# Kernel optimization log

Hardware: AMD Instinct MI355X
Metric: run time of the kernel (lower is better)

## Reference

```python
import jax, jax.numpy as jnp
import numpy as np

HEADS = 5 - 1  # 4 attention heads (GPSConv heads=4)


def _bn(x, g, b, eps=1e-5):
    # BatchNorm1d, training-mode math (biased variance), matches torch normalization
    mu = x.mean(0)
    var = x.var(0)
    return g * (x - mu) * jax.lax.rsqrt(var + eps) + b


def _forward(x, t, freqs, t_fc1_W, t_fc1_b, t_fc2_W, t_fc2_b, node_W, node_b,
             tproj_W, tproj_b, tcat_W, tcat_b, pen_g, pen_b, pel_W, pel_b,
             cat_W, cat_b, conv_Wg, gru_Wih, gru_bih, gru_Whh, gru_bhh,
             attn_Wqkv, attn_bqkv, attn_Wo, attn_bo, bn_g, bn_b,
             mlp_W1, mlp_b1, mlp_W2, mlp_b2, out_W, out_b):
    B, C, Hh, Ww = x.shape
    HD = node_W.shape[1]          # hidden_dim = 64
    DH = HD // HEADS              # per-head dim = 16
    WL = pen_g.shape[0]           # walk_length = 20

    xf = x.reshape(B, -1)                              # [B, D]
    h = xf @ node_W + node_b                           # node_proj

    # TimeEmbedding: t @ freqs -> sin/cos -> MLP, then time_proj
    tp = t.reshape(B, 1) * freqs.reshape(1, -1)        # [B, nf]
    two_pi = jnp.asarray(2.0 * np.pi, x.dtype)
    te = jnp.concatenate([jnp.sin(two_pi * tp), jnp.cos(two_pi * tp)], axis=-1)
    te = jax.nn.silu(te @ t_fc1_W + t_fc1_b) @ t_fc2_W + t_fc2_b
    h_time = te @ tproj_W + tproj_b
    h = jnp.concatenate([h, h_time], axis=-1) @ tcat_W + tcat_b  # time_cat_proj

    # Fully-connected graph incl. self-loops: A = 1 everywhere, deg = B.
    # Random-walk PE: P = A/deg has all entries 1/B; P is idempotent (P@P = P),
    # hence diag(P^k) = diag(P) = 1/B for every k in 1..walk_length.
    A = jnp.ones((B, B), x.dtype)
    P = A / A.sum(1, keepdims=True)
    pe = jnp.broadcast_to(jnp.diagonal(P)[:, None], (B, WL))
    pe = _bn(pe, pen_g, pen_b)                         # pe_norm (batch stats)
    h = jnp.concatenate([h, pe @ pel_W + pel_b], axis=-1) @ cat_W + cat_b

    inv_sqrt = jnp.asarray(1.0 / np.sqrt(DH), x.dtype)
    for l in range(conv_Wg.shape[0]):                  # 5 GPSConv layers
        # --- GatedGraphConv (num_layers=1): message, add-aggregate, GRU ---
        m = A @ (h @ conv_Wg[l])                       # sum of messages from all src nodes
        gi = m @ gru_Wih[l] + gru_bih[l]               # [B, 3H]
        gh = h @ gru_Whh[l] + gru_bhh[l]
        ir, iz, inn = jnp.split(gi, 3, axis=-1)
        hr, hz, hn = jnp.split(gh, 3, axis=-1)
        r = jax.nn.sigmoid(ir + hr)
        z = jax.nn.sigmoid(iz + hz)
        n = jnp.tanh(inn + r * hn)
        hc = (1.0 - z) * n + z * h                     # GRUCell output
        h1 = _bn(hc + h, bn_g[l, 0], bn_b[l, 0])       # residual + norm1

        # --- global multihead self-attention over the single dense batch ---
        qkv = h @ attn_Wqkv[l] + attn_bqkv[l]
        q, k, v = jnp.split(qkv, 3, axis=-1)
        q = q.reshape(B, HEADS, DH).transpose(1, 0, 2)  # [h, B, d]
        k = k.reshape(B, HEADS, DH).transpose(1, 0, 2)
        v = v.reshape(B, HEADS, DH).transpose(1, 0, 2)
        att = jax.nn.softmax(jnp.einsum('hqd,hkd->hqk', q, k) * inv_sqrt, axis=-1)
        o = jnp.einsum('hqk,hkd->hqd', att, v).transpose(1, 0, 2).reshape(B, HD)
        o = o @ attn_Wo[l] + attn_bo[l]
        h2 = _bn(o + h, bn_g[l, 1], bn_b[l, 1])        # residual + norm2

        s = h1 + h2
        s = s + (jax.nn.relu(s @ mlp_W1[l] + mlp_b1[l]) @ mlp_W2[l] + mlp_b2[l])
        h = _bn(s, bn_g[l, 2], bn_b[l, 2])             # norm3

    return (h @ out_W + out_b).reshape(B, C, Hh, Ww)


def setup_inputs() -> dict:
    key = jax.random.key(0)
    B, C, H, W = 2048, 4, 32, 32
    D = C * H * W                 # 4096
    HD, PE, WL, L = 64, 16, 20, 5
    NF, TH, TC = 8, 64, 64
    ks = iter(jax.random.split(key, 40))

    def rn(shape, s=0.05):
        return jax.random.normal(next(ks), shape, jnp.float32) * s

    return {
        'x': jax.random.normal(next(ks), (B, C, H, W), jnp.float32),
        't': jax.random.uniform(next(ks), (B,), jnp.float32),
        'freqs': rn((NF,), 1.0),
        't_fc1_W': rn((2 * NF, TH)), 't_fc1_b': rn((TH,)),
        't_fc2_W': rn((TH, TC)), 't_fc2_b': rn((TC,)),
        'node_W': rn((D, HD), 0.02), 'node_b': rn((HD,)),
        'tproj_W': rn((TC, HD)), 'tproj_b': rn((HD,)),
        'tcat_W': rn((2 * HD, HD)), 'tcat_b': rn((HD,)),
        'pen_g': jnp.ones((WL,), jnp.float32), 'pen_b': jnp.zeros((WL,), jnp.float32),
        'pel_W': rn((WL, PE)), 'pel_b': rn((PE,)),
        'cat_W': rn((HD + PE, HD)), 'cat_b': rn((HD,)),
        'conv_Wg': rn((L, HD, HD)),
        'gru_Wih': rn((L, HD, 3 * HD)), 'gru_bih': rn((L, 3 * HD)),
        'gru_Whh': rn((L, HD, 3 * HD)), 'gru_bhh': rn((L, 3 * HD)),
        'attn_Wqkv': rn((L, HD, 3 * HD)), 'attn_bqkv': rn((L, 3 * HD)),
        'attn_Wo': rn((L, HD, HD)), 'attn_bo': rn((L, HD)),
        'bn_g': jnp.ones((L, 3, HD), jnp.float32), 'bn_b': jnp.zeros((L, 3, HD), jnp.float32),
        'mlp_W1': rn((L, HD, 2 * HD)), 'mlp_b1': rn((L, 2 * HD)),
        'mlp_W2': rn((L, 2 * HD, HD)), 'mlp_b2': rn((L, HD)),
        'out_W': rn((HD, D)), 'out_b': rn((D,)),
    }


def reference(x, t, freqs, t_fc1_W, t_fc1_b, t_fc2_W, t_fc2_b, node_W, node_b,
              tproj_W, tproj_b, tcat_W, tcat_b, pen_g, pen_b, pel_W, pel_b,
              cat_W, cat_b, conv_Wg, gru_Wih, gru_bih, gru_Whh, gru_bhh,
              attn_Wqkv, attn_bqkv, attn_Wo, attn_bo, bn_g, bn_b,
              mlp_W1, mlp_b1, mlp_W2, mlp_b2, out_W, out_b):
    return _forward(x, t, freqs, t_fc1_W, t_fc1_b, t_fc2_W, t_fc2_b, node_W, node_b,
                    tproj_W, tproj_b, tcat_W, tcat_b, pen_g, pen_b, pel_W, pel_b,
                    cat_W, cat_b, conv_Wg, gru_Wih, gru_bih, gru_Whh, gru_bhh,
                    attn_Wqkv, attn_bqkv, attn_Wo, attn_bo, bn_g, bn_b,
                    mlp_W1, mlp_b1, mlp_W2, mlp_b2, out_W, out_b)
```

## Files before the change

kernel.cpp:

```cpp
#include <hip/hip_runtime.h>

#define NB 2048
#define HDM 64
#define NLAY 5
#define NBLK 1024
#define REP 16

#define BAR_U32 (257*32)
#define HSUMR_F  (REP*NLAY*64)
#define BNACCR_F (REP*NLAY*384)

typedef __bf16 bf16x8 __attribute__((ext_vector_type(8)));
typedef float v4f __attribute__((ext_vector_type(4)));

__device__ __forceinline__ float sigmoidf_(float x){ return 1.f/(1.f+__expf(-x)); }
__device__ __forceinline__ float tanhfast_(float x){
  x = fminf(fmaxf(x, -15.f), 15.f);
  float e = __expf(2.f*x);
  return (e-1.f)/(e+1.f);
}
__device__ __forceinline__ unsigned short f2b_rne(float f){
  unsigned u = __float_as_uint(f);
  unsigned r = u + 0x7FFFu + ((u>>16)&1u);
  return (unsigned short)(r>>16);
}
__device__ __forceinline__ unsigned pk2(float a, float b){
  unsigned ua = (__float_as_uint(a) + 0x8000u) >> 16;
  unsigned ub = (__float_as_uint(b) + 0x8000u) & 0xFFFF0000u;
  return ua | ub;
}


__device__ __forceinline__ float ld_f32_sc(const float* p){
  float v;
  asm volatile("global_load_dword %0, %1, off sc0 sc1\n"
               "s_waitcnt vmcnt(0)"
               : "=v"(v) : "v"(p) : "memory");
  return v;
}
__device__ __forceinline__ void ld4_f32_sc(float& a, float& b, float& c, float& d,
                                           const float* p0, const float* p1,
                                           const float* p2, const float* p3){
  asm volatile("global_load_dword %0, %4, off sc0 sc1\n"
               "global_load_dword %1, %5, off sc0 sc1\n"
               "global_load_dword %2, %6, off sc0 sc1\n"
               "global_load_dword %3, %7, off sc0 sc1\n"
               "s_waitcnt vmcnt(0)"
               : "=&v"(a), "=&v"(b), "=&v"(c), "=&v"(d)
               : "v"(p0), "v"(p1), "v"(p2), "v"(p3) : "memory");
}
__device__ __forceinline__ void st_f32_sc(float* p, float v){
  asm volatile("global_store_dword %0, %1, off sc0 sc1" :: "v"(p), "v"(v) : "memory");
}
__device__ __forceinline__ void st_v4f_sc(float* p, v4f v){
  asm volatile("global_store_dwordx4 %0, %1, off sc0 sc1" :: "v"(p), "v"(v) : "memory");
}
__device__ __forceinline__ void st_u16_sc(unsigned short* p, unsigned short v){
  unsigned vv = v;
  asm volatile("global_store_short %0, %1, off sc0 sc1" :: "v"(p), "v"(vv) : "memory");
}


struct KArgs {
  const float *x, *tt, *freqs, *fc1W, *fc1b, *fc2W, *fc2b, *nodeW, *nodeb,
              *tprojW, *tprojb, *tcatW, *tcatb, *penb, *pelW, *pelb, *catW, *catb,
              *convWg, *gruWih, *grubih, *gruWhh, *grubhh, *Wqkv, *bqkv, *Wo, *bo,
              *bng, *bnb, *W1, *b1, *W2, *b2, *outW, *outb;
  float *htime, *hbuf, *s1, *s2, *smlp, *o_out, *h0p, *out;
  float *hsumR, *bnaccR;
  unsigned short *Qb, *Kb, *Vt;
  unsigned *bar;
};

union SMem {
  struct { float xs[16*260]; float tb0[128]; float tb1[128]; } pre;
  struct { float sa[128]; float sb[128]; float cvec[64]; } as;
  struct { float sa[128]; float tot3[128]; } a;
  struct { unsigned short Pl[4*640]; float Os[4*272]; float ms[64]; float ls[64]; } at;
  struct { float sa[128]; float os[128]; float smv[64]; float smT[64]; float sgi[192];
           float Sb1[128]; float Sb2[128]; } b2;
  struct { float sa[128]; float totC[256]; float sh[2*128]; float S2[128]; } c;
  struct { float hsT[64*12]; float totO[128]; } o;
};

__device__ __forceinline__ void gsync(unsigned* base, unsigned round){
  asm volatile("s_waitcnt vmcnt(0)" ::: "memory");
  __syncthreads();
  if (threadIdx.x == 0){
    const unsigned g = (unsigned)blockIdx.x >> 3;
    unsigned* grp   = base + g*32;
    unsigned* glob  = base + 128*32;
    unsigned* flags = base + 129*32;
    unsigned old = __hip_atomic_fetch_add(grp, 1u, __ATOMIC_RELAXED, __HIP_MEMORY_SCOPE_AGENT);
    if ((old & 7u) == 7u){
      unsigned go = __hip_atomic_fetch_add(glob, 1u, __ATOMIC_RELAXED, __HIP_MEMORY_SCOPE_AGENT);
      if ((go & 127u) == 127u){
        #pragma unroll 8
        for (int i=0;i<128;++i)
          __hip_atomic_store(flags + i*32, round+1u, __ATOMIC_RELAXED, __HIP_MEMORY_SCOPE_AGENT);
      }
    }
    unsigned spins = 0u;
    while (__hip_atomic_load(flags + g*32, __ATOMIC_RELAXED, __HIP_MEMORY_SCOPE_AGENT) < round+1u){
      __builtin_amdgcn_s_sleep(8);
      if (++spins > 200000u) break;
    }
    asm volatile("" ::: "memory");
  }
  __syncthreads();
}

__global__ __launch_bounds__(256, 4) void k_fused(KArgs A)
{
  __shared__ SMem sm;
  __shared__ float ghp[2*192];
  const int t = threadIdx.x;
  const int b = blockIdx.x;
  unsigned rnd = 0;

  {
    const int r = t>>6, c = t&63;
    if (r < 2){
      const int row = b*2 + r;
      const float tv = A.tt[row];
      float te[16];
      #pragma unroll
      for (int j=0;j<8;++j){
        float sv, cv;
        __sincosf(6.28318530717958647692f*tv*A.freqs[j], &sv, &cv);
        te[j]=sv; te[j+8]=cv;
      }
      float a = A.fc1b[c];
      #pragma unroll
      for (int j=0;j<16;++j) a += te[j]*A.fc1W[j*64+c];
      sm.pre.tb0[r*64+c] = a*sigmoidf_(a);
    }
    __syncthreads();
    if (r < 2){
      float b2v = A.fc2b[c];
      #pragma unroll 8
      for (int k=0;k<64;++k) b2v += sm.pre.tb0[r*64+k]*A.fc2W[k*64+c];
      sm.pre.tb1[r*64+c] = b2v;
    }
    __syncthreads();
    if (r < 2){
      const int row = b*2 + r;
      float hti = A.tprojb[c];
      #pragma unroll 8
      for (int k=0;k<64;++k) hti += sm.pre.tb1[r*64+k]*A.tprojW[k*64+c];
      A.htime[row*64+c] = hti;
    }
  }
  {
    const int rg = b>>3, kq = b&7;
    const int rows0 = rg*16, k0 = kq*512;
    const int col4 = (t&15)*4;
    const int rq4  = ((t>>4)&3)*4;
    const int ksub = (t>>6)*64;

    float4 a0={0,0,0,0}, a1={0,0,0,0}, a2={0,0,0,0}, a3={0,0,0,0};

    for (int ch=0; ch<2; ++ch){
      __syncthreads();
      #pragma unroll
      for (int i=0;i<4;++i){
        int fi = t + 256*i;
        int xr = fi>>6, kk = (fi&63)<<2;
        *(float4*)&sm.pre.xs[xr*260+kk] =
            *(const float4*)&A.x[(size_t)(rows0+xr)*4096 + k0 + ch*256 + kk];
      }
      __syncthreads();
      const float* wp = &A.nodeW[(size_t)(k0 + ch*256 + ksub)*64 + col4];
      const float* xp = &sm.pre.xs[rq4*260 + ksub];
      #pragma unroll 8
      for (int kk=0; kk<64; ++kk){
        float4 w  = *(const float4*)&wp[kk*64];
        float x0 = xp[kk];
        float x1 = xp[260+kk];
        float x2 = xp[520+kk];
        float x3 = xp[780+kk];
        a0.x += x0*w.x; a0.y += x0*w.y; a0.z += x0*w.z; a0.w += x0*w.w;
        a1.x += x1*w.x; a1.y += x1*w.y; a1.z += x1*w.z; a1.w += x1*w.w;
        a2.x += x2*w.x; a2.y += x2*w.y; a2.z += x2*w.z; a2.w += x2*w.w;
        a3.x += x3*w.x; a3.y += x3*w.y; a3.z += x3*w.z; a3.w += x3*w.w;
      }
    }
    __syncthreads();
    {
      const int kqi = t>>6;
      *(float4*)&sm.pre.xs[(kqi*16 + rq4 + 0)*64 + col4] = a0;
      *(float4*)&sm.pre.xs[(kqi*16 + rq4 + 1)*64 + col4] = a1;
      *(float4*)&sm.pre.xs[(kqi*16 + rq4 + 2)*64 + col4] = a2;
      *(float4*)&sm.pre.xs[(kqi*16 + rq4 + 3)*64 + col4] = a3;
    }
    __syncthreads();
    {
      const int row = t>>4, c4 = (t&15)*4;
      float4 s = {0,0,0,0};
      #pragma unroll
      for (int q=0;q<4;++q){
        float4 v = *(const float4*)&sm.pre.xs[(q*16+row)*64 + c4];
        s.x+=v.x; s.y+=v.y; s.z+=v.z; s.w+=v.w;
      }
      v4f sv = {s.x, s.y, s.z, s.w};
      st_v4f_sc(&A.h0p[(size_t)kq*(NB*HDM) + (rows0+row)*64 + c4], sv);
    }
  }
  gsync(A.bar, rnd++);

  {
    const int r = t>>6, c = t&63;
    const int row = b*2 + r;
    if (r==0){
      float pl[16];
      #pragma unroll
      for (int j=0;j<16;++j){
        float a = A.pelb[j];
        for (int w=0;w<20;++w) a += A.penb[w]*A.pelW[w*16+j];
        pl[j]=a;
      }
      float a = A.catb[c];
      #pragma unroll
      for (int j=0;j<16;++j) a += pl[j]*A.catW[(64+j)*64+c];
      sm.as.cvec[c]=a;
    }
    if (r < 2){
      float p0,p1,p2,p3,p4,p5,p6,p7;
      ld4_f32_sc(p0,p1,p2,p3,
                 &A.h0p[(size_t)0*(NB*HDM) + row*64 + c], &A.h0p[(size_t)1*(NB*HDM) + row*64 + c],
                 &A.h0p[(size_t)2*(NB*HDM) + row*64 + c], &A.h0p[(size_t)3*(NB*HDM) + row*64 + c]);
      ld4_f32_sc(p4,p5,p6,p7,
                 &A.h0p[(size_t)4*(NB*HDM) + row*64 + c], &A.h0p[(size_t)5*(NB*HDM) + row*64 + c],
                 &A.h0p[(size_t)6*(NB*HDM) + row*64 + c], &A.h0p[(size_t)7*(NB*HDM) + row*64 + c]);
      sm.as.sa[t] = A.nodeb[c] + (((p0+p1)+(p2+p3)) + ((p4+p5)+(p6+p7)));
      sm.as.sb[t] = A.htime[row*64+c];
    }
    __syncthreads();
    float a = 0.f;
    if (r < 2){
      a = A.tcatb[c];
      #pragma unroll 4
      for (int k=0;k<64;++k){
        a += sm.as.sa[r*64+k]*A.tcatW[k*64+c];
        a += sm.as.sb[r*64+k]*A.tcatW[(64+k)*64+c];
      }
    }
    __syncthreads();
    if (r < 2) sm.as.sa[t] = a;
    __syncthreads();
    if (r < 2){
      float hv = sm.as.cvec[c];
      #pragma unroll 8
      for (int k=0;k<64;++k) hv += sm.as.sa[r*64+k]*A.catW[k*64+c];
      A.hbuf[row*64+c] = hv;
    }
  }

  for (int l=0; l<NLAY; ++l){
    const float* gPrev = (l==0) ? A.bng : A.bng + (l-1)*192 + 128;
    const float* bPrev = (l==0) ? A.bnb : A.bnb + (l-1)*192 + 128;
    const float* Whh = A.gruWhh + l*12288;
    const float* bhh = A.grubhh + l*192;
    const float* Wq  = A.Wqkv + l*12288;
    const float* bqv = A.bqkv + l*192;
    const int rep = b & (REP-1);

    __syncthreads();
    {
      const int row0 = b*2;
      if (l>0 && t<128){
        float s = 0.f;
        #pragma unroll
        for (int rp=0;rp<REP;++rp) s += A.bnaccR[rp*1920 + (l-1)*384 + 256 + t];
        sm.a.tot3[t] = s;
      }
      __syncthreads();
      if (t < 128){
        const int rl = t>>6, c = t&63;
        const int row = row0 + rl;
        float hv;
        if (l==0){
          hv = A.hbuf[row*64+c];
        } else {
          float mu = sm.a.tot3[c]*(1.f/NB);
          float va = sm.a.tot3[64+c]*(1.f/NB) - mu*mu;
          float sv = ld_f32_sc(&A.smlp[row*64+c]);
          hv = gPrev[c]*(sv-mu)*rsqrtf(va+1e-5f)+bPrev[c];
          A.hbuf[row*64+c] = hv;
        }
        sm.a.sa[t] = hv;
      }
      __syncthreads();
      if (t<64){
        float s = sm.a.sa[t] + sm.a.sa[64+t];
        atomicAdd(&A.hsumR[rep*320 + l*64 + t], s);
      }
      if (t < 192){
        const int cc = t;
        float ag[2], aq[2];
        float bh = bhh[cc], bq_ = bqv[cc];
        ag[0]=bh; ag[1]=bh; aq[0]=bq_; aq[1]=bq_;
        #pragma unroll 4
        for (int k=0;k<64;++k){
          float wh = Whh[k*192+cc];
          float wq = Wq [k*192+cc];
          float h0 = sm.a.sa[k], h1 = sm.a.sa[64+k];
          ag[0] += h0*wh; ag[1] += h1*wh;
          aq[0] += h0*wq; aq[1] += h1*wq;
        }
        ghp[cc]     = ag[0];
        ghp[192+cc] = ag[1];
        #pragma unroll
        for (int rl2=0;rl2<2;++rl2){
          int rw = row0 + rl2;
          float aqv = aq[rl2];
          if (cc < 64){
            int hd = cc>>4, dh = cc&15;
            size_t base = ((size_t)(hd<<11) + rw)*32;
            st_u16_sc(&A.Qb[base+dh], f2b_rne(aqv*0.25f));
            if (l==0) st_u16_sc(&A.Qb[base+16+dh], (unsigned short)0);
          } else if (cc < 128){
            int c2 = cc-64, hd = c2>>4, dh = c2&15;
            size_t base = ((size_t)(hd<<11) + rw)*32;
            st_u16_sc(&A.Kb[base+dh], f2b_rne(aqv));
            if (l==0) st_u16_sc(&A.Kb[base+16+dh], (unsigned short)0);
          } else {
            int c2 = cc-128, hd = c2>>4, dh = c2&15;
            st_u16_sc(&A.Vt[((size_t)(hd*16+dh))*2048 + rw], f2b_rne(aqv));
          }
        }
      }
    }
    gsync(A.bar, rnd++);

    if (b < 512){
      const int w = t>>6, lane = t&63;
      const int q15 = lane & 15, quad = lane >> 4;
      const int qt = b & 127, head = b>>7;
      const int qrow = qt*16 + q15;
      const int key00 = w*512;
      unsigned short* Plw = &sm.at.Pl[w*640];

      const bf16x8 qf = *(const bf16x8*)&A.Qb[(((size_t)(head<<11))+qrow)*32 + quad*8];
      const unsigned short* Kb_h = A.Kb + ((size_t)(head<<11))*32;
      const unsigned short* Vrow = A.Vt + ((size_t)(head*16+q15))*2048;

      v4f O = {0.f,0.f,0.f,0.f};
      float m = -1e30f, lsum = 0.f;

      bf16x8 kf0 = *(const bf16x8*)&Kb_h[(size_t)(key00 + q15)*32 + quad*8];
      bf16x8 kf1 = *(const bf16x8*)&Kb_h[(size_t)(key00 + 16 + q15)*32 + quad*8];
      bf16x8 vf  = *(const bf16x8*)&Vrow[key00 + quad*8];

      for (int c=0; c<16; ++c){
        bf16x8 nk0, nk1, nv;
        if (c < 15){
          int nk = key00 + (c+1)*32;
          nk0 = *(const bf16x8*)&Kb_h[(size_t)(nk + q15)*32 + quad*8];
          nk1 = *(const bf16x8*)&Kb_h[(size_t)(nk + 16 + q15)*32 + quad*8];
          nv  = *(const bf16x8*)&Vrow[nk + quad*8];
        }
        v4f z = {0.f,0.f,0.f,0.f};
        v4f s0 = __builtin_amdgcn_mfma_f32_16x16x32_bf16(kf0, qf, z, 0,0,0);
        v4f s1 = __builtin_amdgcn_mfma_f32_16x16x32_bf16(kf1, qf, z, 0,0,0);
        float cmax = fmaxf(fmaxf(fmaxf(s0[0],s0[1]),fmaxf(s0[2],s0[3])),
                           fmaxf(fmaxf(s1[0],s1[1]),fmaxf(s1[2],s1[3])));
        cmax = fmaxf(cmax, __shfl_xor(cmax,16,64));
        cmax = fmaxf(cmax, __shfl_xor(cmax,32,64));
        float mnew = fmaxf(m, cmax);
        float alpha = __expf(m - mnew);
        float p0=__expf(s0[0]-mnew), p1=__expf(s0[1]-mnew), p2=__expf(s0[2]-mnew), p3=__expf(s0[3]-mnew);
        float p4=__expf(s1[0]-mnew), p5=__expf(s1[1]-mnew), p6=__expf(s1[2]-mnew), p7=__expf(s1[3]-mnew);
        lsum = alpha*lsum + ((p0+p1)+(p2+p3)+((p4+p5)+(p6+p7)));
        m = mnew;
        O[0]*=alpha; O[1]*=alpha; O[2]*=alpha; O[3]*=alpha;
        *(uint2*)&Plw[q15*40 + quad*4]      = make_uint2(pk2(p0,p1), pk2(p2,p3));
        *(uint2*)&Plw[q15*40 + 16 + quad*4] = make_uint2(pk2(p4,p5), pk2(p6,p7));
        asm volatile("s_waitcnt lgkmcnt(0)" ::: "memory");
        bf16x8 pf = *(const bf16x8*)&Plw[q15*40 + quad*8];
        O = __builtin_amdgcn_mfma_f32_16x16x32_bf16(vf, pf, O, 0,0,0);
        kf0 = nk0; kf1 = nk1; vf = nv;
      }
      lsum += __shfl_xor(lsum,16,64);
      lsum += __shfl_xor(lsum,32,64);
      #pragma unroll
      for (int j=0;j<4;++j) sm.at.Os[w*272 + q15*17 + quad*4 + j] = O[j];
      if (quad==0){ sm.at.ms[w*16+q15]=m; sm.at.ls[w*16+q15]=lsum; }
      __syncthreads();
      {
        const int dh = t&15, q = t>>4;
        float m0=sm.at.ms[q], m1=sm.at.ms[16+q], m2=sm.at.ms[32+q], m3=sm.at.ms[48+q];
        float mm = fmaxf(fmaxf(m0,m1),fmaxf(m2,m3));
        float a0=__expf(m0-mm), a1=__expf(m1-mm), a2=__expf(m2-mm), a3=__expf(m3-mm);
        float ll = a0*sm.at.ls[q]+a1*sm.at.ls[16+q]+a2*sm.at.ls[32+q]+a3*sm.at.ls[48+q];
        float oo = a0*sm.at.Os[q*17+dh] + a1*sm.at.Os[272+q*17+dh]
                 + a2*sm.at.Os[544+q*17+dh] + a3*sm.at.Os[816+q*17+dh];
        st_f32_sc(&A.o_out[(size_t)(qt*16+q)*64 + head*16 + dh], oo / ll);
      }
    }
    gsync(A.bar, rnd++);

    {
      const float* Wg  = A.convWg + l*4096;
      const float* Wih = A.gruWih + l*12288;
      const float* bih = A.grubih + l*192;
      const float* WoL = A.Wo + l*4096;
      const float* boL = A.bo + l*64;
      const int row0 = b*2;

      if (t<64){
        float s = 0.f;
        #pragma unroll
        for (int rp=0;rp<REP;++rp) s += A.hsumR[rp*320 + l*64 + t];
        sm.b2.smT[t] = s;
      }
      if (t<128){
        const int rl = t>>6, c = t&63;
        sm.b2.sa[t] = A.hbuf[(size_t)(row0+rl)*64+c];
        sm.b2.os[t] = ld_f32_sc(&A.o_out[(size_t)(row0+rl)*64+c]);
      }
      __syncthreads();
      if (t<64){
        float a=0.f;
        #pragma unroll 8
        for (int k=0;k<64;++k) a += sm.b2.smT[k]*Wg[k*64+t];
        sm.b2.smv[t]=a;
      }
      __syncthreads();
      if (t<192){
        float a = bih[t];
        #pragma unroll 8
        for (int k=0;k<64;++k) a += sm.b2.smv[k]*Wih[k*192+t];
        sm.b2.sgi[t]=a;
      }
      __syncthreads();
      if (t<128){
        const int c = t&63, rg = t>>6;
        float o2 = boL[c];
        #pragma unroll 4
        for (int k=0;k<64;++k) o2 += sm.b2.os[rg*64+k]*WoL[k*64+c];
        const int row = row0 + rg;
        float hv = sm.b2.sa[rg*64+c];
        float s2v = o2 + hv;
        float ir = sm.b2.sgi[c]      + ghp[rg*192+c];
        float iz = sm.b2.sgi[64+c]   + ghp[rg*192+64+c];
        float inn = sm.b2.sgi[128+c];
        float hn  = ghp[rg*192+128+c];
        float rr_ = sigmoidf_(ir);
        float zz  = sigmoidf_(iz);
        float nn  = tanhfast_(inn + rr_*hn);
        float s1v = (1.f-zz)*nn + zz*hv + hv;
        A.s1[(size_t)row*64+c] = s1v;
        A.s2[(size_t)row*64+c] = s2v;
        sm.b2.Sb1[rg*64+c] = s1v;
        sm.b2.Sb2[rg*64+c] = s2v;
      }
      __syncthreads();
      if (t<64){
        float a = sm.b2.Sb1[t] + sm.b2.Sb1[64+t];
        float aq = sm.b2.Sb1[t]*sm.b2.Sb1[t] + sm.b2.Sb1[64+t]*sm.b2.Sb1[64+t];
        float bb = sm.b2.Sb2[t] + sm.b2.Sb2[64+t];
        float bq2 = sm.b2.Sb2[t]*sm.b2.Sb2[t] + sm.b2.Sb2[64+t]*sm.b2.Sb2[64+t];
        float* bl = &A.bnaccR[rep*1920 + l*384];
        atomicAdd(&bl[t],a);      atomicAdd(&bl[64+t],aq);
        atomicAdd(&bl[128+t],bb); atomicAdd(&bl[192+t],bq2);
      }
    }
    gsync(A.bar, rnd++);

    {
      const float* bngL = A.bng + l*192;
      const float* bnbL = A.bnb + l*192;
      const float* W1l = A.W1 + l*8192;
      const float* b1l = A.b1 + l*128;
      const float* W2l = A.W2 + l*8192;
      const float* b2l = A.b2 + l*64;
      const int row0 = b*2;

      {
        float s = 0.f;
        #pragma unroll
        for (int rp=0;rp<REP;++rp) s += A.bnaccR[rp*1920 + l*384 + t];
        sm.c.totC[t] = s;
      }
      __syncthreads();
      if (t<128){
        const int rl = t>>6, c = t&63;
        const int row = row0 + rl;
        float mu1 = sm.c.totC[c]*(1.f/NB);
        float va1 = sm.c.totC[64+c]*(1.f/NB) - mu1*mu1;
        float mu2 = sm.c.totC[128+c]*(1.f/NB);
        float va2 = sm.c.totC[192+c]*(1.f/NB) - mu2*mu2;
        float h1 = bngL[c]*(A.s1[(size_t)row*64+c]-mu1)*rsqrtf(va1+1e-5f)+bnbL[c];
        float h2 = bngL[64+c]*(A.s2[(size_t)row*64+c]-mu2)*rsqrtf(va2+1e-5f)+bnbL[64+c];
        sm.c.sa[t] = h1+h2;
      }
      __syncthreads();
      {
        const int hj = t&127, rgq = t>>7;
        float a0v=b1l[hj];
        #pragma unroll 4
        for (int k=0;k<64;++k) a0v += sm.c.sa[rgq*64+k]*W1l[k*128+hj];
        sm.c.sh[rgq*128+hj] = fmaxf(a0v,0.f);
      }
      __syncthreads();
      if (t<128){
        const int c = t&63, rg = t>>6;
        float mo = b2l[c];
        #pragma unroll 4
        for (int k=0;k<128;++k) mo += sm.c.sh[rg*128+k]*W2l[k*64+c];
        float smv2 = sm.c.sa[rg*64+c] + mo;
        st_f32_sc(&A.smlp[(size_t)(row0+rg)*64+c], smv2);
        sm.c.S2[rg*64+c] = smv2;
      }
      __syncthreads();
      if (t<64){
        float v0 = sm.c.S2[t], v1 = sm.c.S2[64+t];
        float* bl = &A.bnaccR[rep*1920 + l*384];
        atomicAdd(&bl[256+t], v0+v1);
        atomicAdd(&bl[320+t], v0*v0+v1*v1);
      }
    }
    gsync(A.bar, rnd++);
  }

  {
    const float* g4 = A.bng + 896;
    const float* b4 = A.bnb + 896;
    const int rg = b>>2, cg = b&3;
    const int rows0 = rg*8;
    if (t<128){
      float s = 0.f;
      #pragma unroll
      for (int rp=0;rp<REP;++rp) s += A.bnaccR[rp*1920 + 4*384 + 256 + t];
      sm.o.totO[t] = s;
    }
    __syncthreads();
    #pragma unroll
    for (int i=0;i<2;++i){
      int idx = t + 256*i;
      int k = idx&63, rr = idx>>6;
      float sv = ld_f32_sc(&A.smlp[(size_t)(rows0+rr)*64+k]);
      float mu = sm.o.totO[k]*(1.f/NB);
      float va = sm.o.totO[64+k]*(1.f/NB)-mu*mu;
      sm.o.hsT[k*12+rr] = g4[k]*(sv-mu)*rsqrtf(va+1e-5f)+b4[k];
    }
    __syncthreads();
    const int cc = cg*1024 + t*4;
    float4 acc[8];
    {
      float4 bv = *(const float4*)&A.outb[cc];
      #pragma unroll
      for (int rr=0;rr<8;++rr) acc[rr]=bv;
    }
    #pragma unroll 4
    for (int k=0;k<64;++k){
      float4 w = *(const float4*)&A.outW[(size_t)k*4096+cc];
      const float4* hp = (const float4*)&sm.o.hsT[k*12];
      float4 h0=hp[0], h1=hp[1];
      acc[0].x+=h0.x*w.x;  acc[0].y+=h0.x*w.y;  acc[0].z+=h0.x*w.z;  acc[0].w+=h0.x*w.w;
      acc[1].x+=h0.y*w.x;  acc[1].y+=h0.y*w.y;  acc[1].z+=h0.y*w.z;  acc[1].w+=h0.y*w.w;
      acc[2].x+=h0.z*w.x;  acc[2].y+=h0.z*w.y;  acc[2].z+=h0.z*w.z;  acc[2].w+=h0.z*w.w;
      acc[3].x+=h0.w*w.x;  acc[3].y+=h0.w*w.y;  acc[3].z+=h0.w*w.z;  acc[3].w+=h0.w*w.w;
      acc[4].x+=h1.x*w.x;  acc[4].y+=h1.x*w.y;  acc[4].z+=h1.x*w.z;  acc[4].w+=h1.x*w.w;
      acc[5].x+=h1.y*w.x;  acc[5].y+=h1.y*w.y;  acc[5].z+=h1.y*w.z;  acc[5].w+=h1.y*w.w;
      acc[6].x+=h1.z*w.x;  acc[6].y+=h1.z*w.y;  acc[6].z+=h1.z*w.z;  acc[6].w+=h1.z*w.w;
      acc[7].x+=h1.w*w.x;  acc[7].y+=h1.w*w.y;  acc[7].z+=h1.w*w.z;  acc[7].w+=h1.w*w.w;
    }
    #pragma unroll
    for (int rr=0;rr<8;++rr)
      *(float4*)&A.out[(size_t)(rows0+rr)*4096+cc] = acc[rr];
  }
}


extern "C" void kernel_launch(void* const* d_in, const int* in_sizes, int n_in,
                              void* d_out, int out_size, void* d_ws, size_t ws_size,
                              hipStream_t stream)
{
  (void)in_sizes; (void)n_in; (void)out_size; (void)ws_size;
  KArgs A;
  A.x      = (const float*)d_in[0];
  A.tt     = (const float*)d_in[1];
  A.freqs  = (const float*)d_in[2];
  A.fc1W   = (const float*)d_in[3];
  A.fc1b   = (const float*)d_in[4];
  A.fc2W   = (const float*)d_in[5];
  A.fc2b   = (const float*)d_in[6];
  A.nodeW  = (const float*)d_in[7];
  A.nodeb  = (const float*)d_in[8];
  A.tprojW = (const float*)d_in[9];
  A.tprojb = (const float*)d_in[10];
  A.tcatW  = (const float*)d_in[11];
  A.tcatb  = (const float*)d_in[12];
  A.penb   = (const float*)d_in[14];
  A.pelW   = (const float*)d_in[15];
  A.pelb   = (const float*)d_in[16];
  A.catW   = (const float*)d_in[17];
  A.catb   = (const float*)d_in[18];
  A.convWg = (const float*)d_in[19];
  A.gruWih = (const float*)d_in[20];
  A.grubih = (const float*)d_in[21];
  A.gruWhh = (const float*)d_in[22];
  A.grubhh = (const float*)d_in[23];
  A.Wqkv   = (const float*)d_in[24];
  A.bqkv   = (const float*)d_in[25];
  A.Wo     = (const float*)d_in[26];
  A.bo     = (const float*)d_in[27];
  A.bng    = (const float*)d_in[28];
  A.bnb    = (const float*)d_in[29];
  A.W1     = (const float*)d_in[30];
  A.b1     = (const float*)d_in[31];
  A.W2     = (const float*)d_in[32];
  A.b2     = (const float*)d_in[33];
  A.outW   = (const float*)d_in[34];
  A.outb   = (const float*)d_in[35];

  float* ws = (float*)d_ws;
  A.htime = ws;
  A.hbuf  = A.htime + 131072;
  float* ghRegion = A.hbuf + 131072;
  A.s1    = ghRegion + 393216;
  A.s2    = A.s1 + 131072;
  A.smlp  = A.s2 + 131072;
  A.o_out = A.smlp + 131072;
  float* hsum_legacy = A.o_out + 131072;
  float* bnacc_legacy = hsum_legacy + 320;
  A.Qb = (unsigned short*)(bnacc_legacy + 1920);
  A.Kb = A.Qb + 262144;
  unsigned short* vt_legacy = A.Kb + 262144;
  A.h0p  = (float*)(vt_legacy + 65536);
  A.out  = (float*)d_out;

  A.bar    = (unsigned*)ghRegion;
  A.hsumR  = ghRegion + BAR_U32;
  A.bnaccR = A.hsumR + HSUMR_F;
  A.Vt     = (unsigned short*)(A.bnaccR + BNACCR_F);

  hipMemsetAsync(A.bar, 0, (BAR_U32 + HSUMR_F + BNACCR_F)*sizeof(unsigned), stream);
  k_fused<<<dim3(NBLK), dim3(256), 0, stream>>>(A);
}
```

Baseline: 544.6 us.

## Split attention keys across all blocks and replace grid barrier with per-group flags

Attention now runs on all 1024 blocks instead of 512, each block handling half of the keys and writing partial outputs with max and sum stats. The grid-wide barrier between attention and the GRU/out-projection phase is removed. Each block signals a per-query-tile flag and later spins only on the flags of the tiles it needs, then merges the two partial softmax results itself. This aims to halve attention latency per block and drop one global sync per layer. The cost is an extra partial-merge step, more workspace, and a spin-wait with a bounded timeout.

```diff
diff --git a/kernel.cpp b/kernel.cpp
--- a/kernel.cpp
+++ b/kernel.cpp
@@ -9,6 +9,7 @@
 #define BAR_U32 (257*32)
 #define HSUMR_F  (REP*NLAY*64)
 #define BNACCR_F (REP*NLAY*384)
+#define GFLAG_U32 (NLAY*128*32)
 
 typedef __bf16 bf16x8 __attribute__((ext_vector_type(8)));
 typedef float v4f __attribute__((ext_vector_type(4)));
@@ -37,6 +38,13 @@
                "s_waitcnt vmcnt(0)"
                : "=v"(v) : "v"(p) : "memory");
   return v;
+}
+__device__ __forceinline__ void ld2_f32_sc(float& a, float& b,
+                                           const float* p0, const float* p1){
+  asm volatile("global_load_dword %0, %2, off sc0 sc1\n"
+               "global_load_dword %1, %3, off sc0 sc1\n"
+               "s_waitcnt vmcnt(0)"
+               : "=&v"(a), "=&v"(b) : "v"(p0), "v"(p1) : "memory");
 }
 __device__ __forceinline__ void ld4_f32_sc(float& a, float& b, float& c, float& d,
                                            const float* p0, const float* p1,
@@ -66,19 +74,19 @@
               *tprojW, *tprojb, *tcatW, *tcatb, *penb, *pelW, *pelb, *catW, *catb,
               *convWg, *gruWih, *grubih, *gruWhh, *grubhh, *Wqkv, *bqkv, *Wo, *bo,
               *bng, *bnb, *W1, *b1, *W2, *b2, *outW, *outb;
-  float *htime, *hbuf, *s1, *s2, *smlp, *o_out, *h0p, *out;
+  float *htime, *hbuf, *s1, *s2, *smlp, *h0p, *opart, *out;
   float *hsumR, *bnaccR;
   unsigned short *Qb, *Kb, *Vt;
-  unsigned *bar;
+  unsigned *bar, *gflag;
 };
 
 union SMem {
   struct { float xs[16*260]; float tb0[128]; float tb1[128]; } pre;
   struct { float sa[128]; float sb[128]; float cvec[64]; } as;
   struct { float sa[128]; float tot3[128]; } a;
-  struct { unsigned short Pl[4*640]; float Os[4*272]; float ms[64]; float ls[64]; } at;
-  struct { float sa[128]; float os[128]; float smv[64]; float smT[64]; float sgi[192];
-           float Sb1[128]; float Sb2[128]; } b2;
+  struct { unsigned short Pl[4*640]; float Os[4*272]; float ms[64]; float ls[64];
+           float smT[64]; float smv[64]; float sgi[192];
+           float sa2[128]; float Sb1p[128]; float oL2[128]; float Sb2p[128]; } mg;
   struct { float sa[128]; float totC[256]; float sh[2*128]; float S2[128]; } c;
   struct { float hsT[64*12]; float totO[128]; } o;
 };
@@ -263,7 +271,14 @@
     const float* bhh = A.grubhh + l*192;
     const float* Wq  = A.Wqkv + l*12288;
     const float* bqv = A.bqkv + l*192;
+    const float* Wg  = A.convWg + l*4096;
+    const float* Wih = A.gruWih + l*12288;
+    const float* bih = A.grubih + l*192;
+    const float* WoL = A.Wo + l*4096;
+    const float* boL = A.bo + l*64;
     const int rep = b & (REP-1);
+    float* bnaccL = A.bnaccR + rep*1920 + l*384;
+    unsigned* gflagL = A.gflag + l*128*32;
 
     __syncthreads();
     {
@@ -333,13 +348,13 @@
     }
     gsync(A.bar, rnd++);
 
-    if (b < 512){
+    {
+      const int qt = b & 127, head = (b>>7)&3, half = b>>9;
       const int w = t>>6, lane = t&63;
       const int q15 = lane & 15, quad = lane >> 4;
-      const int qt = b & 127, head = b>>7;
       const int qrow = qt*16 + q15;
-      const int key00 = w*512;
-      unsigned short* Plw = &sm.at.Pl[w*640];
+      const int key00 = half*1024 + w*256;
+      unsigned short* Plw = &sm.mg.Pl[w*640];
 
       const bf16x8 qf = *(const bf16x8*)&A.Qb[(((size_t)(head<<11))+qrow)*32 + quad*8];
       const unsigned short* Kb_h = A.Kb + ((size_t)(head<<11))*32;
@@ -352,9 +367,9 @@
       bf16x8 kf1 = *(const bf16x8*)&Kb_h[(size_t)(key00 + 16 + q15)*32 + quad*8];
       bf16x8 vf  = *(const bf16x8*)&Vrow[key00 + quad*8];
 
-      for (int c=0; c<16; ++c){
+      for (int c=0; c<8; ++c){
         bf16x8 nk0, nk1, nv;
-        if (c < 15){
+        if (c < 7){
           int nk = key00 + (c+1)*32;
           nk0 = *(const bf16x8*)&Kb_h[(size_t)(nk + q15)*32 + quad*8];
           nk1 = *(const bf16x8*)&Kb_h[(size_t)(nk + 16 + q15)*32 + quad*8];
@@ -384,86 +399,114 @@
       lsum += __shfl_xor(lsum,16,64);
       lsum += __shfl_xor(lsum,32,64);
       #pragma unroll
-      for (int j=0;j<4;++j) sm.at.Os[w*272 + q15*17 + quad*4 + j] = O[j];
-      if (quad==0){ sm.at.ms[w*16+q15]=m; sm.at.ls[w*16+q15]=lsum; }
+      for (int j=0;j<4;++j) sm.mg.Os[w*272 + q15*17 + quad*4 + j] = O[j];
+      if (quad==0){ sm.mg.ms[w*16+q15]=m; sm.mg.ls[w*16+q15]=lsum; }
       __syncthreads();
       {
         const int dh = t&15, q = t>>4;
-        float m0=sm.at.ms[q], m1=sm.at.ms[16+q], m2=sm.at.ms[32+q], m3=sm.at.ms[48+q];
+        float m0=sm.mg.ms[q], m1=sm.mg.ms[16+q], m2=sm.mg.ms[32+q], m3=sm.mg.ms[48+q];
         float mm = fmaxf(fmaxf(m0,m1),fmaxf(m2,m3));
         float a0=__expf(m0-mm), a1=__expf(m1-mm), a2=__expf(m2-mm), a3=__expf(m3-mm);
-        float ll = a0*sm.at.ls[q]+a1*sm.at.ls[16+q]+a2*sm.at.ls[32+q]+a3*sm.at.ls[48+q];
-        float oo = a0*sm.at.Os[q*17+dh] + a1*sm.at.Os[272+q*17+dh]
-                 + a2*sm.at.Os[544+q*17+dh] + a3*sm.at.Os[816+q*17+dh];
-        st_f32_sc(&A.o_out[(size_t)(qt*16+q)*64 + head*16 + dh], oo / ll);
-      }
-    }
-    gsync(A.bar, rnd++);
-
-    {
-      const float* Wg  = A.convWg + l*4096;
-      const float* Wih = A.gruWih + l*12288;
-      const float* bih = A.grubih + l*192;
-      const float* WoL = A.Wo + l*4096;
-      const float* boL = A.bo + l*64;
-      const int row0 = b*2;
+        float ll = a0*sm.mg.ls[q]+a1*sm.mg.ls[16+q]+a2*sm.mg.ls[32+q]+a3*sm.mg.ls[48+q];
+        float oo = a0*sm.mg.Os[q*17+dh] + a1*sm.mg.Os[272+q*17+dh]
+                 + a2*sm.mg.Os[544+q*17+dh] + a3*sm.mg.Os[816+q*17+dh];
+        float* op = A.opart + (size_t)b*288;
+        st_f32_sc(&op[q*16+dh], oo);
+        if (dh==0){ st_f32_sc(&op[256+q], mm); st_f32_sc(&op[272+q], ll); }
+      }
+      asm volatile("s_waitcnt vmcnt(0)" ::: "memory");
+      __syncthreads();
+      if (t==0)
+        __hip_atomic_fetch_add(gflagL + qt*32, 1u, __ATOMIC_RELAXED, __HIP_MEMORY_SCOPE_AGENT);
 
       if (t<64){
         float s = 0.f;
         #pragma unroll
         for (int rp=0;rp<REP;++rp) s += A.hsumR[rp*320 + l*64 + t];
-        sm.b2.smT[t] = s;
+        sm.mg.smT[t] = s;
       }
       if (t<128){
-        const int rl = t>>6, c = t&63;
-        sm.b2.sa[t] = A.hbuf[(size_t)(row0+rl)*64+c];
-        sm.b2.os[t] = ld_f32_sc(&A.o_out[(size_t)(row0+rl)*64+c]);
+        sm.mg.sa2[t] = A.hbuf[(size_t)(b*2 + (t>>6))*64 + (t&63)];
       }
       __syncthreads();
       if (t<64){
         float a=0.f;
         #pragma unroll 8
-        for (int k=0;k<64;++k) a += sm.b2.smT[k]*Wg[k*64+t];
-        sm.b2.smv[t]=a;
+        for (int k=0;k<64;++k) a += sm.mg.smT[k]*Wg[k*64+t];
+        sm.mg.smv[t]=a;
       }
       __syncthreads();
       if (t<192){
         float a = bih[t];
         #pragma unroll 8
-        for (int k=0;k<64;++k) a += sm.b2.smv[k]*Wih[k*192+t];
-        sm.b2.sgi[t]=a;
+        for (int k=0;k<64;++k) a += sm.mg.smv[k]*Wih[k*192+t];
+        sm.mg.sgi[t]=a;
       }
       __syncthreads();
       if (t<128){
-        const int c = t&63, rg = t>>6;
-        float o2 = boL[c];
-        #pragma unroll 4
-        for (int k=0;k<64;++k) o2 += sm.b2.os[rg*64+k]*WoL[k*64+c];
-        const int row = row0 + rg;
-        float hv = sm.b2.sa[rg*64+c];
-        float s2v = o2 + hv;
-        float ir = sm.b2.sgi[c]      + ghp[rg*192+c];
-        float iz = sm.b2.sgi[64+c]   + ghp[rg*192+64+c];
-        float inn = sm.b2.sgi[128+c];
+        const int rg = t>>6, c = t&63;
+        const int row = b*2 + rg;
+        float hv = sm.mg.sa2[rg*64+c];
+        float ir = sm.mg.sgi[c]      + ghp[rg*192+c];
+        float iz = sm.mg.sgi[64+c]   + ghp[rg*192+64+c];
+        float inn = sm.mg.sgi[128+c];
         float hn  = ghp[rg*192+128+c];
         float rr_ = sigmoidf_(ir);
         float zz  = sigmoidf_(iz);
         float nn  = tanhfast_(inn + rr_*hn);
         float s1v = (1.f-zz)*nn + zz*hv + hv;
         A.s1[(size_t)row*64+c] = s1v;
-        A.s2[(size_t)row*64+c] = s2v;
-        sm.b2.Sb1[rg*64+c] = s1v;
-        sm.b2.Sb2[rg*64+c] = s2v;
+        sm.mg.Sb1p[t] = s1v;
       }
       __syncthreads();
       if (t<64){
-        float a = sm.b2.Sb1[t] + sm.b2.Sb1[64+t];
-        float aq = sm.b2.Sb1[t]*sm.b2.Sb1[t] + sm.b2.Sb1[64+t]*sm.b2.Sb1[64+t];
-        float bb = sm.b2.Sb2[t] + sm.b2.Sb2[64+t];
-        float bq2 = sm.b2.Sb2[t]*sm.b2.Sb2[t] + sm.b2.Sb2[64+t]*sm.b2.Sb2[64+t];
-        float* bl = &A.bnaccR[rep*1920 + l*384];
-        atomicAdd(&bl[t],a);      atomicAdd(&bl[64+t],aq);
-        atomicAdd(&bl[128+t],bb); atomicAdd(&bl[192+t],bq2);
+        float v0 = sm.mg.Sb1p[t], v1 = sm.mg.Sb1p[64+t];
+        atomicAdd(&bnaccL[t],   v0+v1);
+        atomicAdd(&bnaccL[64+t], v0*v0+v1*v1);
+      }
+
+      {
+        const int g = b>>3;
+        if (t==0){
+          unsigned spins = 0u;
+          while (__hip_atomic_load(gflagL + g*32, __ATOMIC_RELAXED, __HIP_MEMORY_SCOPE_AGENT) < 8u){
+            __builtin_amdgcn_s_sleep(4);
+            if (++spins > 400000u) break;
+          }
+        }
+        __syncthreads();
+        if (t<128){
+          const int rg = t>>6, c = t&63;
+          const int head2 = c>>4, dh = c&15;
+          const int row = b*2 + rg, q = row&15, qtr = row>>4;
+          const float* p0 = A.opart + (size_t)(qtr + 128*head2)*288;
+          const float* p1 = p0 + (size_t)512*288;
+          float m0,l0,m1,l1;
+          ld4_f32_sc(m0,l0,m1,l1, &p0[256+q], &p0[272+q], &p1[256+q], &p1[272+q]);
+          float O0,O1;
+          ld2_f32_sc(O0,O1, &p0[q*16+dh], &p1[q*16+dh]);
+          float M = fmaxf(m0,m1);
+          float e0 = __expf(m0-M), e1 = __expf(m1-M);
+          float L = e0*l0 + e1*l1;
+          sm.mg.oL2[rg*64 + c] = (e0*O0 + e1*O1) / L;
+        }
+        __syncthreads();
+        if (t<128){
+          const int rg = t>>6, c = t&63;
+          const int row = b*2 + rg;
+          float o2 = boL[c];
+          #pragma unroll 4
+          for (int k=0;k<64;++k) o2 += sm.mg.oL2[rg*64+k]*WoL[k*64+c];
+          float v = o2 + sm.mg.sa2[rg*64+c];
+          A.s2[(size_t)row*64+c] = v;
+          sm.mg.Sb2p[t] = v;
+        }
+        __syncthreads();
+        if (t<64){
+          float v0 = sm.mg.Sb2p[t], v1 = sm.mg.Sb2p[64+t];
+          atomicAdd(&bnaccL[128+t], v0+v1);
+          atomicAdd(&bnaccL[192+t], v0*v0+v1*v1);
+        }
       }
     }
     gsync(A.bar, rnd++);
@@ -516,9 +559,8 @@
       __syncthreads();
       if (t<64){
         float v0 = sm.c.S2[t], v1 = sm.c.S2[64+t];
-        float* bl = &A.bnaccR[rep*1920 + l*384];
-        atomicAdd(&bl[256+t], v0+v1);
-        atomicAdd(&bl[320+t], v0*v0+v1*v1);
+        atomicAdd(&bnaccL[256+t], v0+v1);
+        atomicAdd(&bnaccL[320+t], v0*v0+v1*v1);
       }
     }
     gsync(A.bar, rnd++);
@@ -623,20 +665,22 @@
   A.s1    = ghRegion + 393216;
   A.s2    = A.s1 + 131072;
   A.smlp  = A.s2 + 131072;
-  A.o_out = A.smlp + 131072;
-  float* hsum_legacy = A.o_out + 131072;
+  float* o_legacy = A.smlp + 131072;
+  float* hsum_legacy = o_legacy + 131072;
   float* bnacc_legacy = hsum_legacy + 320;
   A.Qb = (unsigned short*)(bnacc_legacy + 1920);
   A.Kb = A.Qb + 262144;
   unsigned short* vt_legacy = A.Kb + 262144;
   A.h0p  = (float*)(vt_legacy + 65536);
+  A.opart = A.h0p;
   A.out  = (float*)d_out;
 
   A.bar    = (unsigned*)ghRegion;
   A.hsumR  = ghRegion + BAR_U32;
   A.bnaccR = A.hsumR + HSUMR_F;
-  A.Vt     = (unsigned short*)(A.bnaccR + BNACCR_F);
-
-  hipMemsetAsync(A.bar, 0, (BAR_U32 + HSUMR_F + BNACCR_F)*sizeof(unsigned), stream);
+  A.gflag  = (unsigned*)(A.bnaccR + BNACCR_F);
+  A.Vt     = (unsigned short*)((float*)A.gflag + GFLAG_U32);
+
+  hipMemsetAsync(A.bar, 0, (BAR_U32 + HSUMR_F + BNACCR_F + GFLAG_U32)*sizeof(unsigned), stream);
   k_fused<<<dim3(NBLK), dim3(256), 0, stream>>>(A);
 }
```

New measurement: 913.6 us. 1.68x slower.
